# Kernel tuning notes

Measured on AMD Instinct MI355X. Metric: run time of the kernel, lower is better.

Reference implementation:

```python
import jax, jax.numpy as jnp
import numpy as np

NUM_GRAPHS = 512
EPS_BN = 1e-5


def _bn(x, g, b):
    # BatchNorm1d in training mode: biased batch statistics over node dim
    m = x.mean(0)
    v = x.var(0)
    return g * (x - m) * jax.lax.rsqrt(v + EPS_BN) + b


def _gcn(x, W, b, src, dst):
    # GCNConv with self-loops and symmetric deg^-1/2 normalization
    n = x.shape[0]
    loop = jnp.arange(n, dtype=src.dtype)
    s = jnp.concatenate([src, loop])
    d = jnp.concatenate([dst, loop])
    h = x @ W  # [N, C_out]
    deg = jax.ops.segment_sum(jnp.ones(d.shape[0], dtype=h.dtype), d, num_segments=n)
    dinv = jax.lax.rsqrt(jnp.maximum(deg, 1.0))  # deg >= 1 due to self-loops
    norm = dinv[s] * dinv[d]  # [E+N]
    out = jax.ops.segment_sum(norm[:, None] * h[s], d, num_segments=n)
    return out + b


def setup_inputs() -> dict:
    key = jax.random.key(0)
    ks = jax.random.split(key, 16)
    N, E, F = 100000, 1600000, 6

    def lin(k, fi, fo):
        k1, k2 = jax.random.split(k)
        s = 1.0 / np.sqrt(fi)
        return (jax.random.uniform(k1, (fi, fo), minval=-s, maxval=s),
                jax.random.uniform(k2, (fo,), minval=-s, maxval=s))

    W1, b1 = lin(ks[0], F, 32)
    W2, b2 = lin(ks[1], 32, 64)
    W3, b3 = lin(ks[2], 64, 128)
    Wf1, bf1 = lin(ks[3], 128, 128)
    Wf2, bf2 = lin(ks[4], 128, 64)
    return {
        "x": jax.random.normal(ks[5], (N, F), dtype=jnp.float32),
        "edge_src": jax.random.randint(ks[6], (E,), 0, N, dtype=jnp.int32),
        "edge_dst": jax.random.randint(ks[7], (E,), 0, N, dtype=jnp.int32),
        "batch": jnp.sort(jax.random.randint(ks[8], (N,), 0, NUM_GRAPHS, dtype=jnp.int32)),
        "W1": W1, "b1": b1, "g1": jnp.ones(32), "be1": jnp.zeros(32),
        "W2": W2, "b2": b2, "g2": jnp.ones(64), "be2": jnp.zeros(64),
        "W3": W3, "b3": b3, "g3": jnp.ones(128), "be3": jnp.zeros(128),
        "Wf1": Wf1, "bf1": bf1, "g4": jnp.ones(128), "be4": jnp.zeros(128),
        "Wf2": Wf2, "bf2": bf2,
    }


def reference(x, edge_src, edge_dst, batch,
              W1, b1, g1, be1, W2, b2, g2, be2, W3, b3, g3, be3,
              Wf1, bf1, g4, be4, Wf2, bf2):
    h = jax.nn.relu(_bn(_gcn(x, W1, b1, edge_src, edge_dst), g1, be1))
    h = jax.nn.relu(_bn(_gcn(h, W2, b2, edge_src, edge_dst), g2, be2))
    h = jax.nn.relu(_bn(_gcn(h, W3, b3, edge_src, edge_dst), g3, be3))
    p = jax.ops.segment_max(h, batch, num_segments=NUM_GRAPHS)  # [G, 128]
    p = jax.nn.relu(_bn(p @ Wf1 + bf1, g4, be4))  # dropout = identity (eval)
    p = p @ Wf2 + bf2
    return p / jnp.maximum(jnp.linalg.norm(p, axis=1, keepdims=True), 1e-12)
```

## Files before the change

### kernel.cpp

```cpp
#include <hip/hip_runtime.h>
#include <hip/hip_bf16.h>
#include <hip/hip_fp16.h>

#define NG 512
#define EPS_BN 1e-5f

typedef unsigned short ushort_t;
typedef unsigned int uint_t;

__device__ __forceinline__ float4 f4add(float4 a, float4 b) {
    a.x += b.x; a.y += b.y; a.z += b.z; a.w += b.w; return a;
}
__device__ __forceinline__ float4 f4fma(float s, float4 b, float4 a) {
    a.x = fmaf(s, b.x, a.x); a.y = fmaf(s, b.y, a.y);
    a.z = fmaf(s, b.z, a.z); a.w = fmaf(s, b.w, a.w); return a;
}
__device__ __forceinline__ float4 f4scale(float s, float4 a) {
    a.x *= s; a.y *= s; a.z *= s; a.w *= s; return a;
}
__device__ __forceinline__ float4 bnrelu4(float4 v, float4 sc, float4 sh) {
    float4 r;
    r.x = fmaxf(fmaf(sc.x, v.x, sh.x), 0.f);
    r.y = fmaxf(fmaf(sc.y, v.y, sh.y), 0.f);
    r.z = fmaxf(fmaf(sc.z, v.z, sh.z), 0.f);
    r.w = fmaxf(fmaf(sc.w, v.w, sh.w), 0.f);
    return r;
}
__device__ __forceinline__ void bnparam(float sm, float sq, float ga, float bt,
                                        float invN, float& sc, float& sh) {
    float m = sm * invN;
    float var = fmaf(-m, m, sq * invN);
    sc = ga * rsqrtf(var + EPS_BN);
    sh = fmaf(-m, sc, bt);
}

__device__ __forceinline__ float4 ldh4(const ushort_t* p) {
    uint2 u = *reinterpret_cast<const uint2*>(p);
    __half2 a = *reinterpret_cast<const __half2*>(&u.x);
    __half2 b = *reinterpret_cast<const __half2*>(&u.y);
    float2 fa = __half22float2(a), fb = __half22float2(b);
    float4 r; r.x = fa.x; r.y = fa.y; r.z = fb.x; r.w = fb.y; return r;
}
__device__ __forceinline__ void sth4(ushort_t* p, float4 v) {
    __half2 a = __float22half2_rn(make_float2(v.x, v.y));
    __half2 b = __float22half2_rn(make_float2(v.z, v.w));
    uint2 u;
    u.x = *reinterpret_cast<uint_t*>(&a);
    u.y = *reinterpret_cast<uint_t*>(&b);
    *reinterpret_cast<uint2*>(p) = u;
}


__global__ void k_count(const int* __restrict__ dst, int* __restrict__ cnt, int E) {
    int i = blockIdx.x * blockDim.x + threadIdx.x;
    if (i < E) atomicAdd(&cnt[dst[i]], 1);
}

__global__ void k_dinv(const int* __restrict__ cnt, float* __restrict__ dinv, int N) {
    int i = blockIdx.x * blockDim.x + threadIdx.x;
    if (i < N) dinv[i] = rsqrtf((float)cnt[i] + 1.0f);
}


#define SCAN_T 256
#define SCAN_I 4

__global__ void k_scan1(const int* __restrict__ in, int* __restrict__ out,
                        int* __restrict__ bsum, int N) {
    __shared__ int lds[SCAN_T];
    int t = threadIdx.x;
    int base = blockIdx.x * (SCAN_T * SCAN_I) + t * SCAN_I;
    int v[SCAN_I];
    int sum = 0;
#pragma unroll
    for (int i = 0; i < SCAN_I; ++i) {
        int idx = base + i;
        v[i] = (idx < N) ? in[idx] : 0;
        sum += v[i];
    }
    lds[t] = sum;
    __syncthreads();
    for (int o = 1; o < SCAN_T; o <<= 1) {
        int a = (t >= o) ? lds[t - o] : 0;
        __syncthreads();
        lds[t] += a;
        __syncthreads();
    }
    int run = lds[t] - sum;
#pragma unroll
    for (int i = 0; i < SCAN_I; ++i) {
        int idx = base + i;
        if (idx < N) out[idx] = run;
        run += v[i];
    }
    if (t == SCAN_T - 1) bsum[blockIdx.x] = lds[SCAN_T - 1];
}

__global__ void k_scan2(int* __restrict__ bs, int nb) {
    __shared__ int lds[SCAN_T];
    int t = threadIdx.x;
    int runbase = 0;
    for (int start = 0; start < nb; start += SCAN_T) {
        int idx = start + t;
        int v = (idx < nb) ? bs[idx] : 0;
        lds[t] = v;
        __syncthreads();
        for (int o = 1; o < SCAN_T; o <<= 1) {
            int a = (t >= o) ? lds[t - o] : 0;
            __syncthreads();
            lds[t] += a;
            __syncthreads();
        }
        if (idx < nb) bs[idx] = runbase + lds[t] - v;
        int tot = lds[SCAN_T - 1];
        __syncthreads();
        runbase += tot;
    }
}

__global__ void k_scan3(int* __restrict__ out, const int* __restrict__ bs, int N) {
    int add = bs[blockIdx.x];
    int base = blockIdx.x * (SCAN_T * SCAN_I) + threadIdx.x * SCAN_I;
#pragma unroll
    for (int i = 0; i < SCAN_I; ++i) {
        int idx = base + i;
        if (idx < N) out[idx] += add;
    }
}


__global__ void k_bucket(const int* __restrict__ src, const int* __restrict__ dst,
                         const float* __restrict__ dinv, const int* __restrict__ rowptr,
                         int* __restrict__ fill, int2* __restrict__ e2, int E) {
    int e = blockIdx.x * blockDim.x + threadIdx.x;
    if (e >= E) return;
    int d = dst[e], s = src[e];
    int pos = rowptr[d] + atomicAdd(&fill[d], 1);
    e2[pos] = make_int2(s, __float_as_int(dinv[s]));
}


template <int COUT>
__global__ __launch_bounds__(256) void k_layer1(
    const int* __restrict__ rowptr, const int* __restrict__ cnt,
    const int2* __restrict__ e2, const float* __restrict__ dinv,
    const float* __restrict__ x, const float* __restrict__ W,
    ushort_t* __restrict__ hout, float* __restrict__ sums,
    float* __restrict__ sumsq, int N) {
    constexpr int NPB = 256;
    constexpr int CG = COUT / 4;
    constexpr int RPB = 256 / CG;
    __shared__ float inT[NPB * 6];
    __shared__ float4 wT[6 * CG];
    __shared__ float4 red[256];
    int t = threadIdx.x;
    const float4* W4 = (const float4*)W;
    for (int i = t; i < 6 * CG; i += 256) wT[i] = W4[i];
    int base = blockIdx.x * NPB;
    {
        const float2* x2 = (const float2*)x;
        int ew = t & 3;
        int nl0 = t >> 2;
#pragma unroll 1
        for (int it = 0; it < 4; ++it) {
            int nl = it * 64 + nl0;
            int n = base + nl;
            float a0 = 0, a1 = 0, a2 = 0, a3 = 0, a4 = 0, a5 = 0;
            float di = 0.f;
            if (n < N) {
                di = dinv[n];
                int beg = rowptr[n], end = beg + cnt[n];
                if (ew == 0) {
                    size_t b3 = (size_t)n * 3;
                    float2 p0 = x2[b3], p1 = x2[b3 + 1], p2 = x2[b3 + 2];
                    a0 = di * p0.x; a1 = di * p0.y; a2 = di * p1.x;
                    a3 = di * p1.y; a4 = di * p2.x; a5 = di * p2.y;
                }
                int e = beg + ew;
                for (; e + 4 < end; e += 8) {
                    int2 pa = e2[e], pb = e2[e + 4];
                    size_t sa = (size_t)pa.x * 3, sb = (size_t)pb.x * 3;
                    float2 qa0 = x2[sa], qa1 = x2[sa + 1], qa2 = x2[sa + 2];
                    float2 qb0 = x2[sb], qb1 = x2[sb + 1], qb2 = x2[sb + 2];
                    float wa = __int_as_float(pa.y), wb = __int_as_float(pb.y);
                    a0 = fmaf(wa, qa0.x, a0); a1 = fmaf(wa, qa0.y, a1);
                    a2 = fmaf(wa, qa1.x, a2); a3 = fmaf(wa, qa1.y, a3);
                    a4 = fmaf(wa, qa2.x, a4); a5 = fmaf(wa, qa2.y, a5);
                    a0 = fmaf(wb, qb0.x, a0); a1 = fmaf(wb, qb0.y, a1);
                    a2 = fmaf(wb, qb1.x, a2); a3 = fmaf(wb, qb1.y, a3);
                    a4 = fmaf(wb, qb2.x, a4); a5 = fmaf(wb, qb2.y, a5);
                }
                if (e < end) {
                    int2 pa = e2[e];
                    size_t sa = (size_t)pa.x * 3;
                    float2 qa0 = x2[sa], qa1 = x2[sa + 1], qa2 = x2[sa + 2];
                    float wa = __int_as_float(pa.y);
                    a0 = fmaf(wa, qa0.x, a0); a1 = fmaf(wa, qa0.y, a1);
                    a2 = fmaf(wa, qa1.x, a2); a3 = fmaf(wa, qa1.y, a3);
                    a4 = fmaf(wa, qa2.x, a4); a5 = fmaf(wa, qa2.y, a5);
                }
            }
#pragma unroll
            for (int m = 1; m < 4; m <<= 1) {
                a0 += __shfl_xor(a0, m); a1 += __shfl_xor(a1, m);
                a2 += __shfl_xor(a2, m); a3 += __shfl_xor(a3, m);
                a4 += __shfl_xor(a4, m); a5 += __shfl_xor(a5, m);
            }
            if (ew == 0 && n < N) {
                int o = nl * 6;
                inT[o + 0] = di * a0; inT[o + 1] = di * a1; inT[o + 2] = di * a2;
                inT[o + 3] = di * a3; inT[o + 4] = di * a4; inT[o + 5] = di * a5;
            }
        }
    }
    __syncthreads();
    int gi = t % CG, r0 = t / CG, c0 = gi * 4;
    int nrows = min(NPB, N - base);
    float4 s = {0, 0, 0, 0}, s2 = {0, 0, 0, 0};
    for (int r = r0; r < nrows; r += RPB) {
        const float* row = inT + r * 6;
        float4 acc = {0, 0, 0, 0};
#pragma unroll
        for (int k = 0; k < 6; ++k) acc = f4fma(row[k], wT[k * CG + gi], acc);
        sth4(hout + (size_t)(base + r) * COUT + gi * 4, acc);
        s = f4add(s, acc);
        s2.x = fmaf(acc.x, acc.x, s2.x);
        s2.y = fmaf(acc.y, acc.y, s2.y);
        s2.z = fmaf(acc.z, acc.z, s2.z);
        s2.w = fmaf(acc.w, acc.w, s2.w);
    }
    red[t] = s;
    for (int hh = RPB / 2; hh > 0; hh >>= 1) {
        __syncthreads();
        if (r0 < hh) red[t] = f4add(red[t], red[t + hh * CG]);
    }
    if (r0 == 0) {
        float4 a = red[t];
        atomicAdd(&sums[c0 + 0], a.x); atomicAdd(&sums[c0 + 1], a.y);
        atomicAdd(&sums[c0 + 2], a.z); atomicAdd(&sums[c0 + 3], a.w);
    }
    __syncthreads();
    red[t] = s2;
    for (int hh = RPB / 2; hh > 0; hh >>= 1) {
        __syncthreads();
        if (r0 < hh) red[t] = f4add(red[t], red[t + hh * CG]);
    }
    if (r0 == 0) {
        float4 b = red[t];
        atomicAdd(&sumsq[c0 + 0], b.x); atomicAdd(&sumsq[c0 + 1], b.y);
        atomicAdd(&sumsq[c0 + 2], b.z); atomicAdd(&sumsq[c0 + 3], b.w);
    }
}


template <int CIN, int COUT, int NPB>
__global__ __launch_bounds__(256, 6) void k_layer(
    const int* __restrict__ rowptr, const int* __restrict__ cnt,
    const int2* __restrict__ e2, const float* __restrict__ dinv,
    const ushort_t* __restrict__ hin,
    const float* __restrict__ sums_in, const float* __restrict__ sumsq_in,
    const float* __restrict__ gam, const float* __restrict__ bet,
    const float* __restrict__ W, ushort_t* __restrict__ hout,
    float* __restrict__ sums_out, float* __restrict__ sumsq_out,
    int N, float invN) {
    constexpr int TPN = CIN / 4;
    constexpr int PAD = TPN + 1;
    constexpr int ITER1 = NPB * TPN / 256;
    constexpr int NPI = 256 / TPN;
    constexpr int CG = COUT / 4;
    constexpr int RPB = 256 / CG;
    __shared__ float4 inT4[NPB * PAD];
    __shared__ float4 red[256];
    int t = threadIdx.x;
    const float4* W4 = (const float4*)W;
    int base = blockIdx.x * NPB;
    {
        int c4 = t % TPN;
        float4 sm = reinterpret_cast<const float4*>(sums_in)[c4];
        float4 sq = reinterpret_cast<const float4*>(sumsq_in)[c4];
        float4 ga = reinterpret_cast<const float4*>(gam)[c4];
        float4 bt = reinterpret_cast<const float4*>(bet)[c4];
        float4 sc, sh;
        bnparam(sm.x, sq.x, ga.x, bt.x, invN, sc.x, sh.x);
        bnparam(sm.y, sq.y, ga.y, bt.y, invN, sc.y, sh.y);
        bnparam(sm.z, sq.z, ga.z, bt.z, invN, sc.z, sh.z);
        bnparam(sm.w, sq.w, ga.w, bt.w, invN, sc.w, sh.w);
        const ushort_t* hu = hin;
        int co = c4 * 4;
#pragma unroll
        for (int it = 0; it < ITER1; ++it) {
            int nl = it * NPI + t / TPN;
            int n = base + nl;
            if (n < N) {
                int beg = rowptr[n], end = beg + cnt[n];
                float di = dinv[n];
                float4 acc = f4scale(di, bnrelu4(ldh4(hu + (size_t)n * CIN + co), sc, sh));
                int e = beg;
                if (end - beg >= 4) {
                    int2 p0 = e2[e], p1 = e2[e + 1], p2_ = e2[e + 2], p3_ = e2[e + 3];
                    float4 v0 = ldh4(hu + (size_t)p0.x * CIN + co);
                    float4 v1 = ldh4(hu + (size_t)p1.x * CIN + co);
                    float4 v2 = ldh4(hu + (size_t)p2_.x * CIN + co);
                    float4 v3 = ldh4(hu + (size_t)p3_.x * CIN + co);
                    e += 4;
                    for (; e + 3 < end; e += 4) {
                        int2 q0 = e2[e], q1 = e2[e + 1], q2 = e2[e + 2], q3 = e2[e + 3];
                        float4 w0 = ldh4(hu + (size_t)q0.x * CIN + co);
                        float4 w1 = ldh4(hu + (size_t)q1.x * CIN + co);
                        float4 w2 = ldh4(hu + (size_t)q2.x * CIN + co);
                        float4 w3 = ldh4(hu + (size_t)q3.x * CIN + co);
                        acc = f4fma(__int_as_float(p0.y), bnrelu4(v0, sc, sh), acc);
                        acc = f4fma(__int_as_float(p1.y), bnrelu4(v1, sc, sh), acc);
                        acc = f4fma(__int_as_float(p2_.y), bnrelu4(v2, sc, sh), acc);
                        acc = f4fma(__int_as_float(p3_.y), bnrelu4(v3, sc, sh), acc);
                        p0 = q0; p1 = q1; p2_ = q2; p3_ = q3;
                        v0 = w0; v1 = w1; v2 = w2; v3 = w3;
                    }
                    acc = f4fma(__int_as_float(p0.y), bnrelu4(v0, sc, sh), acc);
                    acc = f4fma(__int_as_float(p1.y), bnrelu4(v1, sc, sh), acc);
                    acc = f4fma(__int_as_float(p2_.y), bnrelu4(v2, sc, sh), acc);
                    acc = f4fma(__int_as_float(p3_.y), bnrelu4(v3, sc, sh), acc);
                }
                for (; e + 1 < end; e += 2) {
                    int2 p0 = e2[e], p1 = e2[e + 1];
                    float4 v0 = ldh4(hu + (size_t)p0.x * CIN + co);
                    float4 v1 = ldh4(hu + (size_t)p1.x * CIN + co);
                    acc = f4fma(__int_as_float(p0.y), bnrelu4(v0, sc, sh), acc);
                    acc = f4fma(__int_as_float(p1.y), bnrelu4(v1, sc, sh), acc);
                }
                if (e < end) {
                    int2 p0 = e2[e];
                    acc = f4fma(__int_as_float(p0.y),
                                bnrelu4(ldh4(hu + (size_t)p0.x * CIN + co), sc, sh), acc);
                }
                inT4[nl * PAD + c4] = f4scale(di, acc);
            }
        }
    }
    __syncthreads();
    int gi = t % CG, r0 = t / CG, c0 = gi * 4;
    int nrows = min(NPB, N - base);
    float4 s = {0, 0, 0, 0}, s2 = {0, 0, 0, 0};
    for (int r = r0; r < nrows; r += RPB) {
        const float* row = (const float*)(inT4 + r * PAD);
        float4 acc = {0, 0, 0, 0};
#pragma unroll 8
        for (int k = 0; k < CIN; ++k) acc = f4fma(row[k], W4[k * CG + gi], acc);
        sth4(hout + (size_t)(base + r) * COUT + gi * 4, acc);
        s = f4add(s, acc);
        s2.x = fmaf(acc.x, acc.x, s2.x);
        s2.y = fmaf(acc.y, acc.y, s2.y);
        s2.z = fmaf(acc.z, acc.z, s2.z);
        s2.w = fmaf(acc.w, acc.w, s2.w);
    }
    red[t] = s;
    for (int hh = RPB / 2; hh > 0; hh >>= 1) {
        __syncthreads();
        if (r0 < hh) red[t] = f4add(red[t], red[t + hh * CG]);
    }
    if (r0 == 0) {
        float4 a = red[t];
        atomicAdd(&sums_out[c0 + 0], a.x); atomicAdd(&sums_out[c0 + 1], a.y);
        atomicAdd(&sums_out[c0 + 2], a.z); atomicAdd(&sums_out[c0 + 3], a.w);
    }
    __syncthreads();
    red[t] = s2;
    for (int hh = RPB / 2; hh > 0; hh >>= 1) {
        __syncthreads();
        if (r0 < hh) red[t] = f4add(red[t], red[t + hh * CG]);
    }
    if (r0 == 0) {
        float4 b = red[t];
        atomicAdd(&sumsq_out[c0 + 0], b.x); atomicAdd(&sumsq_out[c0 + 1], b.y);
        atomicAdd(&sumsq_out[c0 + 2], b.z); atomicAdd(&sumsq_out[c0 + 3], b.w);
    }
}


template <int CIN, int COUT, int ROWS>
__global__ __launch_bounds__(256) void k_mm_stats(
    const float* __restrict__ in, const float* __restrict__ W,
    float* __restrict__ out, float* __restrict__ sums,
    float* __restrict__ sumsq, int N) {
    constexpr int CG = COUT / 4;
    constexpr int RPB = 256 / CG;
    __shared__ float4 inT4[ROWS * CIN / 4];
    float* inT = (float*)inT4;
    __shared__ float4 wT[CIN * CG];
    __shared__ float4 red[256];
    int t = threadIdx.x;
    const float4* W4 = reinterpret_cast<const float4*>(W);
    for (int i = t; i < CIN * CG; i += 256) wT[i] = W4[i];
    int base = blockIdx.x * ROWS;
    int nrows = min(ROWS, N - base);
    {
        const float4* in4 = reinterpret_cast<const float4*>(in + (size_t)base * CIN);
        int tot = nrows * (CIN / 4);
        for (int i = t; i < tot; i += 256) inT4[i] = in4[i];
    }
    __syncthreads();
    int gi = t % CG, r0 = t / CG, c0 = gi * 4;
    float4 s = {0, 0, 0, 0}, s2 = {0, 0, 0, 0};
    for (int r = r0; r < nrows; r += RPB) {
        const float* row = inT + r * CIN;
        float4 acc = {0, 0, 0, 0};
#pragma unroll
        for (int k = 0; k < CIN; ++k) acc = f4fma(row[k], wT[k * CG + gi], acc);
        reinterpret_cast<float4*>(out + (size_t)(base + r) * COUT)[gi] = acc;
        s = f4add(s, acc);
        s2.x = fmaf(acc.x, acc.x, s2.x);
        s2.y = fmaf(acc.y, acc.y, s2.y);
        s2.z = fmaf(acc.z, acc.z, s2.z);
        s2.w = fmaf(acc.w, acc.w, s2.w);
    }
    red[t] = s;
    for (int hh = RPB / 2; hh > 0; hh >>= 1) {
        __syncthreads();
        if (r0 < hh) red[t] = f4add(red[t], red[t + hh * CG]);
    }
    if (r0 == 0) {
        float4 a = red[t];
        atomicAdd(&sums[c0 + 0], a.x); atomicAdd(&sums[c0 + 1], a.y);
        atomicAdd(&sums[c0 + 2], a.z); atomicAdd(&sums[c0 + 3], a.w);
    }
    __syncthreads();
    red[t] = s2;
    for (int hh = RPB / 2; hh > 0; hh >>= 1) {
        __syncthreads();
        if (r0 < hh) red[t] = f4add(red[t], red[t + hh * CG]);
    }
    if (r0 == 0) {
        float4 b = red[t];
        atomicAdd(&sumsq[c0 + 0], b.x); atomicAdd(&sumsq[c0 + 1], b.y);
        atomicAdd(&sumsq[c0 + 2], b.z); atomicAdd(&sumsq[c0 + 3], b.w);
    }
}


__global__ void k_segmax_bn(const ushort_t* __restrict__ h, const int* __restrict__ batch,
                            const float* __restrict__ sums, const float* __restrict__ sumsq,
                            const float* __restrict__ gam, const float* __restrict__ bet,
                            float* __restrict__ pool, int N, float invN) {
    int t = threadIdx.x;
    int c = t & 127;
    int sub = t >> 7;
    int base = blockIdx.x * 64 + sub * 32;
    if (base >= N) return;
    float sc, sh;
    bnparam(sums[c], sumsq[c], gam[c], bet[c], invN, sc, sh);
    int cur = batch[base];
    float h0 = __half2float(*reinterpret_cast<const __half*>(&h[(size_t)base * 128 + c]));
    float mx = fmaxf(fmaf(sc, h0, sh), 0.f);
    int lim = min(32, N - base);
    for (int i = 1; i < lim; ++i) {
        int n = base + i;
        int b = batch[n];
        float hv = __half2float(*reinterpret_cast<const __half*>(&h[(size_t)n * 128 + c]));
        float v = fmaxf(fmaf(sc, hv, sh), 0.f);
        if (b != cur) {
            atomicMax(reinterpret_cast<int*>(pool) + (cur << 7) + c, __float_as_int(mx));
            cur = b; mx = v;
        } else {
            mx = fmaxf(mx, v);
        }
    }
    atomicMax(reinterpret_cast<int*>(pool) + (cur << 7) + c, __float_as_int(mx));
}


__global__ void k_head(const float* __restrict__ Z, const float* __restrict__ sums,
                       const float* __restrict__ sumsq, const float* __restrict__ gam,
                       const float* __restrict__ bet, const float* __restrict__ Wf2,
                       const float* __restrict__ bf2, float* __restrict__ out) {
    int g = blockIdx.x, c = threadIdx.x;
    __shared__ float row[128];
    const float invG = 1.0f / (float)NG;
    for (int j = c; j < 128; j += 64) {
        float sc, sh;
        bnparam(sums[j], sumsq[j], gam[j], bet[j], invG, sc, sh);
        row[j] = fmaxf(fmaf(sc, Z[(g << 7) + j], sh), 0.f);
    }
    __syncthreads();
    float acc = bf2[c];
#pragma unroll
    for (int k = 0; k < 128; ++k) acc = fmaf(row[k], Wf2[k * 64 + c], acc);
    float ss = acc * acc;
#pragma unroll
    for (int off = 32; off; off >>= 1) ss += __shfl_xor(ss, off);
    out[(g << 6) + c] = acc / fmaxf(sqrtf(ss), 1e-12f);
}


extern "C" void kernel_launch(void* const* d_in, const int* in_sizes, int n_in,
                              void* d_out, int out_size, void* d_ws, size_t ws_size,
                              hipStream_t stream) {
    const float* x    = (const float*)d_in[0];
    const int*   src  = (const int*)d_in[1];
    const int*   dst  = (const int*)d_in[2];
    const int*   batch= (const int*)d_in[3];
    const float* W1   = (const float*)d_in[4];
    const float* g1   = (const float*)d_in[6];
    const float* be1  = (const float*)d_in[7];
    const float* W2   = (const float*)d_in[8];
    const float* g2   = (const float*)d_in[10];
    const float* be2  = (const float*)d_in[11];
    const float* W3   = (const float*)d_in[12];
    const float* g3   = (const float*)d_in[14];
    const float* be3  = (const float*)d_in[15];
    const float* Wf1  = (const float*)d_in[16];
    const float* g4   = (const float*)d_in[18];
    const float* be4  = (const float*)d_in[19];
    const float* Wf2  = (const float*)d_in[20];
    const float* bf2  = (const float*)d_in[21];
    float* out = (float*)d_out;

    const int N = in_sizes[0] / 6;
    const int E = in_sizes[1];
    const int nScanBlocks = (N + SCAN_T * SCAN_I - 1) / (SCAN_T * SCAN_I);

    char* ws = (char*)d_ws;
    size_t off = 0;
    auto carve = [&](size_t bytes) {
        void* p = ws + off;
        off += (bytes + 255) & ~(size_t)255;
        return p;
    };
    int*     cnt    = (int*)carve((size_t)N * 4);
    float*   dinv   = (float*)carve((size_t)N * 4);
    int*     rowptr = (int*)carve((size_t)N * 4);
    int*     fill   = (int*)carve((size_t)N * 4);
    int*     bsum   = (int*)carve((size_t)4096 * 4);
    int2*    e2     = (int2*)carve((size_t)E * 8);
    ushort_t* H1    = (ushort_t*)carve((size_t)N * 32 * 2);
    ushort_t* H2    = (ushort_t*)carve((size_t)N * 64 * 2);
    ushort_t* H3    = (ushort_t*)carve((size_t)N * 128 * 2);
    float*   stats  = (float*)carve(704 * 4);
    float*   pool   = (float*)carve((size_t)NG * 128 * 4);
    float*   Z      = (float*)carve((size_t)NG * 128 * 4);
    float* s1 = stats;
    float* s2 = stats + 64;
    float* s3 = stats + 192;
    float* s4 = stats + 448;

    const float invN = 1.0f / (float)N;

    hipMemsetAsync(cnt, 0, (size_t)N * 4, stream);
    hipMemsetAsync(fill, 0, (size_t)N * 4, stream);
    hipMemsetAsync(stats, 0, 704 * 4, stream);
    hipMemsetAsync(pool, 0, (size_t)NG * 128 * 4, stream);
    k_count<<<(E + 255) / 256, 256, 0, stream>>>(dst, cnt, E);
    k_dinv<<<(N + 255) / 256, 256, 0, stream>>>(cnt, dinv, N);
    k_scan1<<<nScanBlocks, SCAN_T, 0, stream>>>(cnt, rowptr, bsum, N);
    k_scan2<<<1, SCAN_T, 0, stream>>>(bsum, nScanBlocks);
    k_scan3<<<nScanBlocks, SCAN_T, 0, stream>>>(rowptr, bsum, N);
    k_bucket<<<(E + 255) / 256, 256, 0, stream>>>(src, dst, dinv, rowptr, fill, e2, E);

    k_layer1<32><<<(N + 255) / 256, 256, 0, stream>>>(
        rowptr, cnt, e2, dinv, x, W1, H1, s1, s1 + 32, N);

    k_layer<32, 64, 64><<<(N + 63) / 64, 256, 0, stream>>>(
        rowptr, cnt, e2, dinv, H1, s1, s1 + 32, g1, be1, W2, H2,
        s2, s2 + 64, N, invN);

    k_layer<64, 128, 64><<<(N + 63) / 64, 256, 0, stream>>>(
        rowptr, cnt, e2, dinv, H2, s2, s2 + 64, g2, be2, W3, H3,
        s3, s3 + 128, N, invN);

    k_segmax_bn<<<(N + 63) / 64, 256, 0, stream>>>(H3, batch, s3, s3 + 128, g3, be3, pool, N, invN);

    k_mm_stats<128, 128, 64><<<(NG + 63) / 64, 256, 0, stream>>>(pool, Wf1, Z, s4, s4 + 128, NG);
    k_head<<<NG, 64, 0, stream>>>(Z, s4, s4 + 128, g4, be4, Wf2, bf2, out);
}
```

Before: 776.5 us.

## Stage per-block CSR edge lists in LDS and deepen gather batching

Each block first copies its contiguous range of (src, weight) edge pairs from global memory into a shared-memory buffer. The aggregation loops then read edge indices from LDS instead of repeatedly hitting global memory, with a fallback global path when a block's edge range overflows the buffer. The k_layer gather loop is unrolled to issue 8 feature loads before a sched_barrier, and the occupancy hint drops from 6 to 4 waves to make room for the extra registers and LDS. The costs are an extra block-wide sync, larger LDS use per block and lower occupancy, which may reduce latency hiding for the random feature gathers.

```diff
diff --git a/kernel.cpp b/kernel.cpp
--- a/kernel.cpp
+++ b/kernel.cpp
@@ -150,13 +150,24 @@
     constexpr int NPB = 256;
     constexpr int CG = COUT / 4;
     constexpr int RPB = 256 / CG;
+    constexpr int ECAP1 = 4608;
     __shared__ float inT[NPB * 6];
     __shared__ float4 wT[6 * CG];
     __shared__ float4 red[256];
+    __shared__ int2 eLDS[ECAP1];
     int t = threadIdx.x;
     const float4* W4 = (const float4*)W;
     for (int i = t; i < 6 * CG; i += 256) wT[i] = W4[i];
     int base = blockIdx.x * NPB;
+    int lastn = min(base + NPB, N) - 1;
+    int eBeg = rowptr[base];
+    int eEnd = rowptr[lastn] + cnt[lastn];
+    int M = eEnd - eBeg;
+    bool useL = (M <= ECAP1);
+    if (useL) {
+        for (int i = t; i < M; i += 256) eLDS[i] = e2[eBeg + i];
+    }
+    __syncthreads();
     {
         const float2* x2 = (const float2*)x;
         int ew = t & 3;
@@ -176,28 +187,41 @@
                     a0 = di * p0.x; a1 = di * p0.y; a2 = di * p1.x;
                     a3 = di * p1.y; a4 = di * p2.x; a5 = di * p2.y;
                 }
-                int e = beg + ew;
-                for (; e + 4 < end; e += 8) {
-                    int2 pa = e2[e], pb = e2[e + 4];
-                    size_t sa = (size_t)pa.x * 3, sb = (size_t)pb.x * 3;
-                    float2 qa0 = x2[sa], qa1 = x2[sa + 1], qa2 = x2[sa + 2];
-                    float2 qb0 = x2[sb], qb1 = x2[sb + 1], qb2 = x2[sb + 2];
-                    float wa = __int_as_float(pa.y), wb = __int_as_float(pb.y);
-                    a0 = fmaf(wa, qa0.x, a0); a1 = fmaf(wa, qa0.y, a1);
-                    a2 = fmaf(wa, qa1.x, a2); a3 = fmaf(wa, qa1.y, a3);
-                    a4 = fmaf(wa, qa2.x, a4); a5 = fmaf(wa, qa2.y, a5);
-                    a0 = fmaf(wb, qb0.x, a0); a1 = fmaf(wb, qb0.y, a1);
-                    a2 = fmaf(wb, qb1.x, a2); a3 = fmaf(wb, qb1.y, a3);
-                    a4 = fmaf(wb, qb2.x, a4); a5 = fmaf(wb, qb2.y, a5);
-                }
-                if (e < end) {
-                    int2 pa = e2[e];
-                    size_t sa = (size_t)pa.x * 3;
-                    float2 qa0 = x2[sa], qa1 = x2[sa + 1], qa2 = x2[sa + 2];
-                    float wa = __int_as_float(pa.y);
-                    a0 = fmaf(wa, qa0.x, a0); a1 = fmaf(wa, qa0.y, a1);
-                    a2 = fmaf(wa, qa1.x, a2); a3 = fmaf(wa, qa1.y, a3);
-                    a4 = fmaf(wa, qa2.x, a4); a5 = fmaf(wa, qa2.y, a5);
+                if (useL) {
+                    int r = beg - eBeg + ew, re = end - eBeg;
+                    for (; r + 4 < re; r += 8) {
+                        int2 pa = eLDS[r], pb = eLDS[r + 4];
+                        size_t sa = (size_t)pa.x * 3, sb = (size_t)pb.x * 3;
+                        float2 qa0 = x2[sa], qa1 = x2[sa + 1], qa2 = x2[sa + 2];
+                        float2 qb0 = x2[sb], qb1 = x2[sb + 1], qb2 = x2[sb + 2];
+                        __builtin_amdgcn_sched_barrier(0);
+                        float wa = __int_as_float(pa.y), wb = __int_as_float(pb.y);
+                        a0 = fmaf(wa, qa0.x, a0); a1 = fmaf(wa, qa0.y, a1);
+                        a2 = fmaf(wa, qa1.x, a2); a3 = fmaf(wa, qa1.y, a3);
+                        a4 = fmaf(wa, qa2.x, a4); a5 = fmaf(wa, qa2.y, a5);
+                        a0 = fmaf(wb, qb0.x, a0); a1 = fmaf(wb, qb0.y, a1);
+                        a2 = fmaf(wb, qb1.x, a2); a3 = fmaf(wb, qb1.y, a3);
+                        a4 = fmaf(wb, qb2.x, a4); a5 = fmaf(wb, qb2.y, a5);
+                    }
+                    if (r < re) {
+                        int2 pa = eLDS[r];
+                        size_t sa = (size_t)pa.x * 3;
+                        float2 qa0 = x2[sa], qa1 = x2[sa + 1], qa2 = x2[sa + 2];
+                        float wa = __int_as_float(pa.y);
+                        a0 = fmaf(wa, qa0.x, a0); a1 = fmaf(wa, qa0.y, a1);
+                        a2 = fmaf(wa, qa1.x, a2); a3 = fmaf(wa, qa1.y, a3);
+                        a4 = fmaf(wa, qa2.x, a4); a5 = fmaf(wa, qa2.y, a5);
+                    }
+                } else {
+                    for (int e = beg + ew; e < end; e += 4) {
+                        int2 pa = e2[e];
+                        size_t sa = (size_t)pa.x * 3;
+                        float2 qa0 = x2[sa], qa1 = x2[sa + 1], qa2 = x2[sa + 2];
+                        float wa = __int_as_float(pa.y);
+                        a0 = fmaf(wa, qa0.x, a0); a1 = fmaf(wa, qa0.y, a1);
+                        a2 = fmaf(wa, qa1.x, a2); a3 = fmaf(wa, qa1.y, a3);
+                        a4 = fmaf(wa, qa2.x, a4); a5 = fmaf(wa, qa2.y, a5);
+                    }
                 }
             }
 #pragma unroll
@@ -254,7 +278,7 @@
 
 
 template <int CIN, int COUT, int NPB>
-__global__ __launch_bounds__(256, 6) void k_layer(
+__global__ __launch_bounds__(256, 4) void k_layer(
     const int* __restrict__ rowptr, const int* __restrict__ cnt,
     const int2* __restrict__ e2, const float* __restrict__ dinv,
     const ushort_t* __restrict__ hin,
@@ -269,11 +293,22 @@
     constexpr int NPI = 256 / TPN;
     constexpr int CG = COUT / 4;
     constexpr int RPB = 256 / CG;
+    constexpr int ECAP = 2048;
     __shared__ float4 inT4[NPB * PAD];
     __shared__ float4 red[256];
+    __shared__ int2 eLDS[ECAP];
     int t = threadIdx.x;
     const float4* W4 = (const float4*)W;
     int base = blockIdx.x * NPB;
+    int lastn = min(base + NPB, N) - 1;
+    int eBeg = rowptr[base];
+    int eEnd = rowptr[lastn] + cnt[lastn];
+    int M = eEnd - eBeg;
+    bool useL = (M <= ECAP);
+    if (useL) {
+        for (int i = t; i < M; i += 256) eLDS[i] = e2[eBeg + i];
+    }
+    __syncthreads();
     {
         int c4 = t % TPN;
         float4 sm = reinterpret_cast<const float4*>(sums_in)[c4];
@@ -295,43 +330,55 @@
                 int beg = rowptr[n], end = beg + cnt[n];
                 float di = dinv[n];
                 float4 acc = f4scale(di, bnrelu4(ldh4(hu + (size_t)n * CIN + co), sc, sh));
-                int e = beg;
-                if (end - beg >= 4) {
-                    int2 p0 = e2[e], p1 = e2[e + 1], p2_ = e2[e + 2], p3_ = e2[e + 3];
-                    float4 v0 = ldh4(hu + (size_t)p0.x * CIN + co);
-                    float4 v1 = ldh4(hu + (size_t)p1.x * CIN + co);
-                    float4 v2 = ldh4(hu + (size_t)p2_.x * CIN + co);
-                    float4 v3 = ldh4(hu + (size_t)p3_.x * CIN + co);
-                    e += 4;
-                    for (; e + 3 < end; e += 4) {
-                        int2 q0 = e2[e], q1 = e2[e + 1], q2 = e2[e + 2], q3 = e2[e + 3];
-                        float4 w0 = ldh4(hu + (size_t)q0.x * CIN + co);
-                        float4 w1 = ldh4(hu + (size_t)q1.x * CIN + co);
-                        float4 w2 = ldh4(hu + (size_t)q2.x * CIN + co);
-                        float4 w3 = ldh4(hu + (size_t)q3.x * CIN + co);
+                if (useL) {
+                    int r = beg - eBeg, re = end - eBeg;
+                    for (; r + 7 < re; r += 8) {
+                        int2 p0 = eLDS[r],     p1 = eLDS[r + 1];
+                        int2 p2_ = eLDS[r + 2], p3_ = eLDS[r + 3];
+                        int2 p4 = eLDS[r + 4], p5 = eLDS[r + 5];
+                        int2 p6 = eLDS[r + 6], p7 = eLDS[r + 7];
+                        float4 v0 = ldh4(hu + (size_t)p0.x * CIN + co);
+                        float4 v1 = ldh4(hu + (size_t)p1.x * CIN + co);
+                        float4 v2 = ldh4(hu + (size_t)p2_.x * CIN + co);
+                        float4 v3 = ldh4(hu + (size_t)p3_.x * CIN + co);
+                        float4 v4 = ldh4(hu + (size_t)p4.x * CIN + co);
+                        float4 v5 = ldh4(hu + (size_t)p5.x * CIN + co);
+                        float4 v6 = ldh4(hu + (size_t)p6.x * CIN + co);
+                        float4 v7 = ldh4(hu + (size_t)p7.x * CIN + co);
+                        __builtin_amdgcn_sched_barrier(0);
                         acc = f4fma(__int_as_float(p0.y), bnrelu4(v0, sc, sh), acc);
                         acc = f4fma(__int_as_float(p1.y), bnrelu4(v1, sc, sh), acc);
                         acc = f4fma(__int_as_float(p2_.y), bnrelu4(v2, sc, sh), acc);
                         acc = f4fma(__int_as_float(p3_.y), bnrelu4(v3, sc, sh), acc);
-                        p0 = q0; p1 = q1; p2_ = q2; p3_ = q3;
-                        v0 = w0; v1 = w1; v2 = w2; v3 = w3;
+                        acc = f4fma(__int_as_float(p4.y), bnrelu4(v4, sc, sh), acc);
+                        acc = f4fma(__int_as_float(p5.y), bnrelu4(v5, sc, sh), acc);
+                        acc = f4fma(__int_as_float(p6.y), bnrelu4(v6, sc, sh), acc);
+                        acc = f4fma(__int_as_float(p7.y), bnrelu4(v7, sc, sh), acc);
                     }
-                    acc = f4fma(__int_as_float(p0.y), bnrelu4(v0, sc, sh), acc);
-                    acc = f4fma(__int_as_float(p1.y), bnrelu4(v1, sc, sh), acc);
-                    acc = f4fma(__int_as_float(p2_.y), bnrelu4(v2, sc, sh), acc);
-                    acc = f4fma(__int_as_float(p3_.y), bnrelu4(v3, sc, sh), acc);
-                }
-                for (; e + 1 < end; e += 2) {
-                    int2 p0 = e2[e], p1 = e2[e + 1];
-                    float4 v0 = ldh4(hu + (size_t)p0.x * CIN + co);
-                    float4 v1 = ldh4(hu + (size_t)p1.x * CIN + co);
-                    acc = f4fma(__int_as_float(p0.y), bnrelu4(v0, sc, sh), acc);
-                    acc = f4fma(__int_as_float(p1.y), bnrelu4(v1, sc, sh), acc);
-                }
-                if (e < end) {
-                    int2 p0 = e2[e];
-                    acc = f4fma(__int_as_float(p0.y),
-                                bnrelu4(ldh4(hu + (size_t)p0.x * CIN + co), sc, sh), acc);
+                    for (; r + 3 < re; r += 4) {
+                        int2 p0 = eLDS[r], p1 = eLDS[r + 1];
+                        int2 p2_ = eLDS[r + 2], p3_ = eLDS[r + 3];
+                        float4 v0 = ldh4(hu + (size_t)p0.x * CIN + co);
+                        float4 v1 = ldh4(hu + (size_t)p1.x * CIN + co);
+                        float4 v2 = ldh4(hu + (size_t)p2_.x * CIN + co);
+                        float4 v3 = ldh4(hu + (size_t)p3_.x * CIN + co);
+                        __builtin_amdgcn_sched_barrier(0);
+                        acc = f4fma(__int_as_float(p0.y), bnrelu4(v0, sc, sh), acc);
+                        acc = f4fma(__int_as_float(p1.y), bnrelu4(v1, sc, sh), acc);
+                        acc = f4fma(__int_as_float(p2_.y), bnrelu4(v2, sc, sh), acc);
+                        acc = f4fma(__int_as_float(p3_.y), bnrelu4(v3, sc, sh), acc);
+                    }
+                    for (; r < re; ++r) {
+                        int2 p0 = eLDS[r];
+                        acc = f4fma(__int_as_float(p0.y),
+                                    bnrelu4(ldh4(hu + (size_t)p0.x * CIN + co), sc, sh), acc);
+                    }
+                } else {
+                    for (int e = beg; e < end; ++e) {
+                        int2 p0 = e2[e];
+                        acc = f4fma(__int_as_float(p0.y),
+                                    bnrelu4(ldh4(hu + (size_t)p0.x * CIN + co), sc, sh), acc);
+                    }
                 }
                 inT4[nl * PAD + c4] = f4scale(di, acc);
             }
```

Measured after the change: 751.5 us (median of 2 runs). -3.2%, faster.
